# Performance work log

Measured on AMD Instinct MI355X. Metric: run time of the kernel, lower is better.

## Reference

```python
import jax, jax.numpy as jnp
import numpy as np

N, F_IN, F_OUT = 2048, 128, 64


def setup_inputs() -> dict:
    key = jax.random.key(0)
    k0, k1, k2, k3, k4 = jax.random.split(key, 5)
    node_features = jax.random.normal(k0, (N, F_IN), dtype=jnp.float32)
    adjacency_matrix = jax.random.uniform(k1, (N, N), dtype=jnp.float32)
    mask_father = jax.random.uniform(k2, (N, N), dtype=jnp.float32)
    mask_hadamard = jax.random.uniform(k3, (N, N), dtype=jnp.float32)
    # kaiming_uniform (fan_in, relu): bound = sqrt(6 / fan_in) * sqrt(2) adjustment -> gain*sqrt(3/fan_in)
    bound = np.sqrt(2.0) * np.sqrt(3.0 / F_IN)
    weight = jax.random.uniform(k4, (F_IN, F_OUT), dtype=jnp.float32, minval=-bound, maxval=bound)
    bias = jnp.zeros((F_OUT,), dtype=jnp.float32)
    return {
        "node_features": node_features,
        "adjacency_matrix": adjacency_matrix,
        "mask_father": mask_father,
        "mask_hadamard": mask_hadamard,
        "weight": weight,
        "bias": bias,
    }


def reference(node_features, adjacency_matrix, mask_father, mask_hadamard, weight, bias):
    # H[i,f] = (X @ W + b)[i,f]
    H = node_features @ weight + bias  # [N, F]
    # Original math: out[j,f] = sum_k mf[j,k] * H[k,f] * (sum_i A[j,i] * H[i,f] * mh[i,k])
    # G[j,f,k] corresponds to the (masked hadamard @ adjacency) intermediate [N, F, N]
    G = jnp.einsum('ji,if,ik->jfk', adjacency_matrix, H, mask_hadamard)
    out = jnp.einsum('jfk,kf,jk->jf', G, H, mask_father)
    return out
```

## Files before the change

### kernel.cpp

```cpp
#include <hip/hip_runtime.h>
#include <hip/hip_bf16.h>


typedef __attribute__((ext_vector_type(8))) _Float16 f16x8;
typedef __attribute__((ext_vector_type(4))) _Float16 f16x4;
typedef __attribute__((ext_vector_type(16))) float f32x16;

#define N 2048
#define FOUT 64
#define FIN 128
#define NIT 512

#define ZERO16 ((f32x16){0.f,0.f,0.f,0.f,0.f,0.f,0.f,0.f,0.f,0.f,0.f,0.f,0.f,0.f,0.f,0.f})
#define MFMA32(A,B,C) __builtin_amdgcn_mfma_f32_32x32x16_f16((A),(B),(C),0,0,0)

__device__ __forceinline__ void gl_lds16(const _Float16* g, _Float16* l) {
    __builtin_amdgcn_global_load_lds(
        (const __attribute__((address_space(1))) void*)g,
        (__attribute__((address_space(3))) void*)l, 16, 0, 0);
}


__global__ __launch_bounds__(256) void k_h(const float* __restrict__ X,
                                           const float* __restrict__ W,
                                           const float* __restrict__ bias,
                                           float* __restrict__ HT,
                                           _Float16* __restrict__ HTh) {
    __shared__ float Ws[FIN * FOUT];
    __shared__ float Xs[4 * FIN];
    int t = threadIdx.x;
#pragma unroll
    for (int s = 0; s < 32; ++s) Ws[t + 256 * s] = W[t + 256 * s];
    int i0 = blockIdx.x * 4;
#pragma unroll
    for (int s = 0; s < 2; ++s) { int idx = t + 256 * s; Xs[idx] = X[(size_t)i0 * FIN + idx]; }
    __syncthreads();
    int f = t & 63, il = t >> 6;
    float h = bias[f];
#pragma unroll
    for (int p = 0; p < FIN; ++p) h = fmaf(Xs[il * FIN + p], Ws[p * FOUT + f], h);
    int i = i0 + il;
    HT[f * N + i] = h;
    HTh[f * N + i] = (_Float16)h;
}

__global__ __launch_bounds__(256) void k_a2h(const float* __restrict__ A,
                                             _Float16* __restrict__ Ah) {
    int g = blockIdx.x * 256 + threadIdx.x;
    float4 v = ((const float4*)A)[g];
    f16x4 o;
    o[0] = (_Float16)v.x; o[1] = (_Float16)v.y; o[2] = (_Float16)v.z; o[3] = (_Float16)v.w;
    ((f16x4*)Ah)[g] = o;
}

__global__ __launch_bounds__(256) void k_mht(const float* __restrict__ mh,
                                             _Float16* __restrict__ mhT) {
    __shared__ float tile[64][65];
    int t = threadIdx.x;
    int bx = blockIdx.x & 31;
    int by = blockIdx.x >> 5;
#pragma unroll
    for (int s = 0; s < 16; ++s) {
        int lin = t + 256 * s;
        int r = lin >> 6, c = lin & 63;
        tile[r][c] = mh[(size_t)(by * 64 + r) * N + bx * 64 + c];
    }
    __syncthreads();
#pragma unroll
    for (int s = 0; s < 16; ++s) {
        int lin = t + 256 * s;
        int kr = lin >> 6, ic = lin & 63;
        mhT[(size_t)(bx * 64 + kr) * N + by * 64 + ic] = (_Float16)tile[ic][kr];
    }
}


#define STAGE(DBUF, IT)                                                        \
  {                                                                            \
    int ib_ = ((IT) & 31) << 6;                                                \
    int kt_ = (IT) >> 5;                                                       \
    const char* gA_ = (const char*)Ah + ((size_t)jbase * N + ib_) * 2;         \
    const char* gB_ = (const char*)mhT + ((size_t)kt_ * 128 * N + ib_) * 2;    \
    _Float16* la_ = &tiles[DBUF][0][lds_w];                                    \
    _Float16* lb_ = &tiles[DBUF][1][lds_w];                                    \
    _Pragma("unroll")                                                          \
    for (int c_ = 0; c_ < 4; ++c_) {                                           \
      gl_lds16((const _Float16*)(gA_ + (size_t)c_ * (16 * N) + vbyte), la_ + c_ * 512); \
      gl_lds16((const _Float16*)(gB_ + (size_t)c_ * (16 * N) + vbyte), lb_ + c_ * 512); \
    }                                                                          \
  }

#define COMPUTE_HALF(BUF, IT)                                                  \
  {                                                                            \
    const char* hb_ = (const char*)hbuf + ((((IT) & 31) << 6) * 2);            \
    __builtin_amdgcn_s_setprio(1);                                             \
    _Pragma("unroll")                                                          \
    for (int ks = 0; ks < 4; ++ks) {                                           \
      f16x8 a0 = *(const f16x8*)(tbase + addrA[ks] + (BUF) * 32768);           \
      f16x8 a1 = *(const f16x8*)(tbase + addrA[ks] + (BUF) * 32768 + 4096);    \
      f16x8 b0 = *(const f16x8*)(tbase + addrB[ks] + (BUF) * 32768 + 16384);   \
      f16x8 b1 = *(const f16x8*)(tbase + addrB[ks] + (BUF) * 32768 + 20480);   \
      f16x8 h0 = *(const f16x8*)(hb_ + hlb + ks * 32);                         \
      f16x8 h1 = *(const f16x8*)(hb_ + hlb + 4096 + ks * 32);                  \
      f16x8 a00 = a0 * h0, a10 = a1 * h0, a01 = a0 * h1, a11 = a1 * h1;        \
      acc[0][0][0] = MFMA32(a00, b0, acc[0][0][0]);                            \
      acc[0][0][1] = MFMA32(a00, b1, acc[0][0][1]);                            \
      acc[0][1][0] = MFMA32(a10, b0, acc[0][1][0]);                            \
      acc[0][1][1] = MFMA32(a10, b1, acc[0][1][1]);                            \
      acc[1][0][0] = MFMA32(a01, b0, acc[1][0][0]);                            \
      acc[1][0][1] = MFMA32(a01, b1, acc[1][0][1]);                            \
      acc[1][1][0] = MFMA32(a11, b0, acc[1][1][0]);                            \
      acc[1][1][1] = MFMA32(a11, b1, acc[1][1][1]);                            \
    }                                                                          \
    __builtin_amdgcn_s_setprio(0);                                             \
  }

#define EPILOGUE(IT)                                                           \
  {                                                                            \
    int kb_ = (((IT) >> 5) << 7) + wk;                                         \
    float hk0[2], hk1[2];                                                      \
    _Pragma("unroll")                                                          \
    for (int tk = 0; tk < 2; ++tk) {                                           \
      int kg = kb_ + tk * 32 + l31;                                            \
      hk0[tk] = HT[f0 * N + kg];                                               \
      hk1[tk] = HT[(f0 + 1) * N + kg];                                         \
    }                                                                          \
    _Pragma("unroll")                                                          \
    for (int tj = 0; tj < 2; ++tj) {                                           \
      int jr0 = jbase + wj + tj * 32 + hi * 4;                                 \
      _Pragma("unroll")                                                        \
      for (int r = 0; r < 16; ++r) {                                           \
        int jr = jr0 + (r & 3) + 8 * (r >> 2);                                 \
        float s0 = 0.f, s1 = 0.f;                                              \
        _Pragma("unroll")                                                      \
        for (int tk = 0; tk < 2; ++tk) {                                       \
          int kg = kb_ + tk * 32 + l31;                                        \
          float m = mf[(size_t)jr * N + kg];                                   \
          s0 = fmaf(acc[0][tj][tk][r], m * hk0[tk], s0);                       \
          s1 = fmaf(acc[1][tj][tk][r], m * hk1[tk], s1);                       \
        }                                                                      \
        s0 += __shfl_xor(s0, 1);  s1 += __shfl_xor(s1, 1);                     \
        s0 += __shfl_xor(s0, 2);  s1 += __shfl_xor(s1, 2);                     \
        s0 += __shfl_xor(s0, 4);  s1 += __shfl_xor(s1, 4);                     \
        s0 += __shfl_xor(s0, 8);  s1 += __shfl_xor(s1, 8);                     \
        s0 += __shfl_xor(s0, 16); s1 += __shfl_xor(s1, 16);                    \
        if (l31 == 0) {                                                        \
          int slot = tj * 32 + (r & 3) + 8 * (r >> 2) + 4 * hi;                \
          red[0][w][slot] += s0;                                               \
          red[1][w][slot] += s1;                                               \
        }                                                                      \
      }                                                                        \
    }                                                                          \
    _Pragma("unroll")                                                          \
    for (int f_ = 0; f_ < 2; ++f_)                                             \
      _Pragma("unroll")                                                        \
      for (int a_ = 0; a_ < 2; ++a_)                                           \
        _Pragma("unroll")                                                      \
        for (int b_ = 0; b_ < 2; ++b_) acc[f_][a_][b_] = ZERO16;               \
  }

__global__ __launch_bounds__(256, 2) void k_main(const float* __restrict__ mf,
                                                 const float* __restrict__ HT,
                                                 const _Float16* __restrict__ HTh,
                                                 const _Float16* __restrict__ Ah,
                                                 const _Float16* __restrict__ mhT,
                                                 float* __restrict__ out) {
    __shared__ _Float16 tiles[2][2][128 * 64];
    __shared__ _Float16 hbuf[2][N];
    __shared__ float red[2][4][64];

    int t = threadIdx.x;
    int jbase = (blockIdx.x >> 5) << 7;
    int f0 = (blockIdx.x & 31) << 1;
    int w = t >> 6, lane = t & 63;
    int l31 = lane & 31, hi = lane >> 5, l7 = lane & 7;
    int wj = (w & 1) << 6, wk = (w >> 1) << 6;

#pragma unroll
    for (int s = 0; s < 2; ++s) {
        int idx = t + 256 * s;
        ((f16x8*)hbuf)[idx] = *(const f16x8*)&HTh[(size_t)(f0 + (idx >> 8)) * N + (idx & 255) * 8];
    }
    ((float*)red)[t] = 0.f;
    ((float*)red)[t + 256] = 0.f;

    int lrow = lane >> 3;
    int lchunk = (lane & 7) ^ lrow;
    int vbyte = ((w * 32 + lrow) * N + lchunk * 8) * 2;
    int lds_w = w * 2048;

    const char* tbase = (const char*)&tiles[0][0][0];
    int hlb = hi * 16;
    int addrA[4], addrB[4];
#pragma unroll
    for (int ks = 0; ks < 4; ++ks) {
        int chs = ((ks * 2 + hi) ^ l7) * 16;
        addrA[ks] = (wj + l31) * 128 + chs;
        addrB[ks] = (wk + l31) * 128 + chs;
    }

    STAGE(0, 0)

    f32x16 acc[2][2][2];
#pragma unroll
    for (int f_ = 0; f_ < 2; ++f_)
#pragma unroll
        for (int a_ = 0; a_ < 2; ++a_)
#pragma unroll
            for (int b_ = 0; b_ < 2; ++b_) acc[f_][a_][b_] = ZERO16;

    for (int tp = 0; tp < NIT / 2; ++tp) {
        int it0 = tp * 2;
        __syncthreads();
        STAGE(1, it0 + 1)
        COMPUTE_HALF(0, it0)
        __syncthreads();
        if (tp != NIT / 2 - 1) STAGE(0, it0 + 2)
        COMPUTE_HALF(1, it0 + 1)
        if (((it0 + 1) & 31) == 31) EPILOGUE(it0 + 1)
    }

    __syncthreads();
    if (t < 128) {
        int j = t;
#pragma unroll
        for (int fi = 0; fi < 2; ++fi) {
            float v = (j < 64) ? (red[fi][0][j] + red[fi][2][j])
                               : (red[fi][1][j - 64] + red[fi][3][j - 64]);
            out[(size_t)(jbase + j) * FOUT + f0 + fi] = v;
        }
    }
}

extern "C" void kernel_launch(void* const* d_in, const int* in_sizes, int n_in,
                              void* d_out, int out_size, void* d_ws, size_t ws_size,
                              hipStream_t stream) {
    const float* X    = (const float*)d_in[0];
    const float* A    = (const float*)d_in[1];
    const float* mf   = (const float*)d_in[2];
    const float* mh   = (const float*)d_in[3];
    const float* W    = (const float*)d_in[4];
    const float* bias = (const float*)d_in[5];
    float* out = (float*)d_out;

    float*    HT  = (float*)d_ws;
    _Float16* HTh = (_Float16*)((char*)d_ws + 524288);
    _Float16* Ah  = (_Float16*)((char*)d_ws + 1048576);
    _Float16* mhT = (_Float16*)((char*)d_ws + 1048576 + 8388608);

    k_h<<<N / 4, 256, 0, stream>>>(X, W, bias, HT, HTh);
    k_a2h<<<(N * N / 4) / 256, 256, 0, stream>>>(A, Ah);
    k_mht<<<(N / 64) * (N / 64), 256, 0, stream>>>(mh, mhT);
    k_main<<<16 * 32, 256, 0, stream>>>(mf, HT, HTh, Ah, mhT, out);
}
```

Measured before the change: 1.253 ms.

## Split k range across blocks with atomics and switch to 16x16x32 MFMA tiles

The main kernel's k dimension is split in half across twice as many blocks, and partial outputs are combined with atomicAdd into an output that a new kernel zeroes first. The inner loop moves from 32x32x16 MFMAs with 64-wide i tiles to 16x16x32 MFMAs with 32-wide i tiles, halving LDS tile size, and the swizzles and epilogue reduction are reworked to match. The goal is more blocks across the CUs and a lighter LDS footprint, at the cost of an extra launch, atomics, and more MFMA instructions per unit of work.

```diff
diff --git a/kernel.cpp b/kernel.cpp
--- a/kernel.cpp
+++ b/kernel.cpp
@@ -4,15 +4,14 @@
 
 typedef __attribute__((ext_vector_type(8))) _Float16 f16x8;
 typedef __attribute__((ext_vector_type(4))) _Float16 f16x4;
-typedef __attribute__((ext_vector_type(16))) float f32x16;
+typedef __attribute__((ext_vector_type(4))) float f32x4;
 
 #define N 2048
 #define FOUT 64
 #define FIN 128
 #define NIT 512
 
-#define ZERO16 ((f32x16){0.f,0.f,0.f,0.f,0.f,0.f,0.f,0.f,0.f,0.f,0.f,0.f,0.f,0.f,0.f,0.f})
-#define MFMA32(A,B,C) __builtin_amdgcn_mfma_f32_32x32x16_f16((A),(B),(C),0,0,0)
+#define MFMA16(A,B,C) __builtin_amdgcn_mfma_f32_16x16x32_f16((A),(B),(C),0,0,0)
 
 __device__ __forceinline__ void gl_lds16(const _Float16* g, _Float16* l) {
     __builtin_amdgcn_global_load_lds(
@@ -20,6 +19,10 @@
         (__attribute__((address_space(3))) void*)l, 16, 0, 0);
 }
 
+
+__global__ __launch_bounds__(256) void k_zero(float* __restrict__ out) {
+    ((float4*)out)[blockIdx.x * 256 + threadIdx.x] = make_float4(0.f, 0.f, 0.f, 0.f);
+}
 
 __global__ __launch_bounds__(256) void k_h(const float* __restrict__ X,
                                            const float* __restrict__ W,
@@ -77,86 +80,86 @@
 
 #define STAGE(DBUF, IT)                                                        \
   {                                                                            \
-    int ib_ = ((IT) & 31) << 6;                                                \
-    int kt_ = (IT) >> 5;                                                       \
-    const char* gA_ = (const char*)Ah + ((size_t)jbase * N + ib_) * 2;         \
-    const char* gB_ = (const char*)mhT + ((size_t)kt_ * 128 * N + ib_) * 2;    \
-    _Float16* la_ = &tiles[DBUF][0][lds_w];                                    \
-    _Float16* lb_ = &tiles[DBUF][1][lds_w];                                    \
-    _Pragma("unroll")                                                          \
-    for (int c_ = 0; c_ < 4; ++c_) {                                           \
-      gl_lds16((const _Float16*)(gA_ + (size_t)c_ * (16 * N) + vbyte), la_ + c_ * 512); \
-      gl_lds16((const _Float16*)(gB_ + (size_t)c_ * (16 * N) + vbyte), lb_ + c_ * 512); \
+    int ib_ = ((IT) & 63) << 5;                                                \
+    int kt_ = (IT) >> 6;                                                       \
+    const _Float16* pa_ = Ah + a_base + ib_;                                   \
+    const _Float16* pb_ = mhT + b_base + (size_t)kt_ * 128 * N + ib_;          \
+    _Float16* la_ = &tiles[DBUF][0][w * 1024];                                 \
+    _Float16* lb_ = &tiles[DBUF][1][w * 1024];                                 \
+    _Pragma("unroll")                                                          \
+    for (int c_ = 0; c_ < 2; ++c_) {                                           \
+      gl_lds16(pa_ + c_ * 16 * N, la_ + c_ * 512);                             \
+      gl_lds16(pb_ + c_ * 16 * N, lb_ + c_ * 512);                             \
     }                                                                          \
   }
 
 #define COMPUTE_HALF(BUF, IT)                                                  \
   {                                                                            \
-    const char* hb_ = (const char*)hbuf + ((((IT) & 31) << 6) * 2);            \
+    const char* hb_ = (const char*)hbuf + (((IT) & 63) << 6);                  \
+    f16x8 ar[4], br[4];                                                        \
+    _Pragma("unroll")                                                          \
+    for (int x_ = 0; x_ < 4; ++x_)                                             \
+      ar[x_] = *(const f16x8*)(tbase + (BUF) * 16384 + faA + x_ * 1024);       \
+    _Pragma("unroll")                                                          \
+    for (int x_ = 0; x_ < 4; ++x_)                                             \
+      br[x_] = *(const f16x8*)(tbase + (BUF) * 16384 + 8192 + faB + x_ * 1024);\
+    f16x8 h0 = *(const f16x8*)(hb_ + hq);                                      \
+    f16x8 h1 = *(const f16x8*)(hb_ + 4096 + hq);                               \
     __builtin_amdgcn_s_setprio(1);                                             \
     _Pragma("unroll")                                                          \
-    for (int ks = 0; ks < 4; ++ks) {                                           \
-      f16x8 a0 = *(const f16x8*)(tbase + addrA[ks] + (BUF) * 32768);           \
-      f16x8 a1 = *(const f16x8*)(tbase + addrA[ks] + (BUF) * 32768 + 4096);    \
-      f16x8 b0 = *(const f16x8*)(tbase + addrB[ks] + (BUF) * 32768 + 16384);   \
-      f16x8 b1 = *(const f16x8*)(tbase + addrB[ks] + (BUF) * 32768 + 20480);   \
-      f16x8 h0 = *(const f16x8*)(hb_ + hlb + ks * 32);                         \
-      f16x8 h1 = *(const f16x8*)(hb_ + hlb + 4096 + ks * 32);                  \
-      f16x8 a00 = a0 * h0, a10 = a1 * h0, a01 = a0 * h1, a11 = a1 * h1;        \
-      acc[0][0][0] = MFMA32(a00, b0, acc[0][0][0]);                            \
-      acc[0][0][1] = MFMA32(a00, b1, acc[0][0][1]);                            \
-      acc[0][1][0] = MFMA32(a10, b0, acc[0][1][0]);                            \
-      acc[0][1][1] = MFMA32(a10, b1, acc[0][1][1]);                            \
-      acc[1][0][0] = MFMA32(a01, b0, acc[1][0][0]);                            \
-      acc[1][0][1] = MFMA32(a01, b1, acc[1][0][1]);                            \
-      acc[1][1][0] = MFMA32(a11, b0, acc[1][1][0]);                            \
-      acc[1][1][1] = MFMA32(a11, b1, acc[1][1][1]);                            \
+    for (int jj = 0; jj < 4; ++jj) {                                           \
+      f16x8 a0 = ar[jj] * h0;                                                  \
+      f16x8 a1 = ar[jj] * h1;                                                  \
+      _Pragma("unroll")                                                        \
+      for (int kk = 0; kk < 4; ++kk) {                                         \
+        acc[0][jj][kk] = MFMA16(a0, br[kk], acc[0][jj][kk]);                   \
+        acc[1][jj][kk] = MFMA16(a1, br[kk], acc[1][jj][kk]);                   \
+      }                                                                        \
     }                                                                          \
     __builtin_amdgcn_s_setprio(0);                                             \
+    if (((IT) & 63) == 63) EPILOGUE(IT)                                        \
   }
 
 #define EPILOGUE(IT)                                                           \
   {                                                                            \
-    int kb_ = (((IT) >> 5) << 7) + wk;                                         \
-    float hk0[2], hk1[2];                                                      \
-    _Pragma("unroll")                                                          \
-    for (int tk = 0; tk < 2; ++tk) {                                           \
-      int kg = kb_ + tk * 32 + l31;                                            \
-      hk0[tk] = HT[f0 * N + kg];                                               \
-      hk1[tk] = HT[(f0 + 1) * N + kg];                                         \
+    int kb_ = khalf + (((IT) >> 6) << 7);                                      \
+    _Pragma("unroll")                                                          \
+    for (int jj = 0; jj < 4; ++jj) {                                           \
+      float t0[4] = {0.f, 0.f, 0.f, 0.f};                                      \
+      float t1[4] = {0.f, 0.f, 0.f, 0.f};                                      \
+      int jrow = jbase + wj + jj * 16 + q * 4;                                 \
+      _Pragma("unroll")                                                        \
+      for (int kk = 0; kk < 4; ++kk) {                                         \
+        int kg = kb_ + wk + kk * 16 + l16;                                     \
+        float hk0 = HT[f0 * N + kg];                                           \
+        float hk1 = HT[(f0 + 1) * N + kg];                                     \
+        _Pragma("unroll")                                                      \
+        for (int r = 0; r < 4; ++r) {                                          \
+          float m = mf[(size_t)(jrow + r) * N + kg];                           \
+          t0[r] = fmaf(acc[0][jj][kk][r], m * hk0, t0[r]);                     \
+          t1[r] = fmaf(acc[1][jj][kk][r], m * hk1, t1[r]);                     \
+        }                                                                      \
+      }                                                                        \
+      _Pragma("unroll")                                                        \
+      for (int r = 0; r < 4; ++r) {                                            \
+        float v0 = t0[r], v1 = t1[r];                                          \
+        v0 += __shfl_xor(v0, 1); v1 += __shfl_xor(v1, 1);                      \
+        v0 += __shfl_xor(v0, 2); v1 += __shfl_xor(v1, 2);                      \
+        v0 += __shfl_xor(v0, 4); v1 += __shfl_xor(v1, 4);                      \
+        v0 += __shfl_xor(v0, 8); v1 += __shfl_xor(v1, 8);                      \
+        if (l16 == 0) {                                                        \
+          red[0][w][jj * 16 + q * 4 + r] += v0;                                \
+          red[1][w][jj * 16 + q * 4 + r] += v1;                                \
+        }                                                                      \
+      }                                                                        \
     }                                                                          \
     _Pragma("unroll")                                                          \
-    for (int tj = 0; tj < 2; ++tj) {                                           \
-      int jr0 = jbase + wj + tj * 32 + hi * 4;                                 \
-      _Pragma("unroll")                                                        \
-      for (int r = 0; r < 16; ++r) {                                           \
-        int jr = jr0 + (r & 3) + 8 * (r >> 2);                                 \
-        float s0 = 0.f, s1 = 0.f;                                              \
-        _Pragma("unroll")                                                      \
-        for (int tk = 0; tk < 2; ++tk) {                                       \
-          int kg = kb_ + tk * 32 + l31;                                        \
-          float m = mf[(size_t)jr * N + kg];                                   \
-          s0 = fmaf(acc[0][tj][tk][r], m * hk0[tk], s0);                       \
-          s1 = fmaf(acc[1][tj][tk][r], m * hk1[tk], s1);                       \
-        }                                                                      \
-        s0 += __shfl_xor(s0, 1);  s1 += __shfl_xor(s1, 1);                     \
-        s0 += __shfl_xor(s0, 2);  s1 += __shfl_xor(s1, 2);                     \
-        s0 += __shfl_xor(s0, 4);  s1 += __shfl_xor(s1, 4);                     \
-        s0 += __shfl_xor(s0, 8);  s1 += __shfl_xor(s1, 8);                     \
-        s0 += __shfl_xor(s0, 16); s1 += __shfl_xor(s1, 16);                    \
-        if (l31 == 0) {                                                        \
-          int slot = tj * 32 + (r & 3) + 8 * (r >> 2) + 4 * hi;                \
-          red[0][w][slot] += s0;                                               \
-          red[1][w][slot] += s1;                                               \
-        }                                                                      \
-      }                                                                        \
-    }                                                                          \
-    _Pragma("unroll")                                                          \
-    for (int f_ = 0; f_ < 2; ++f_)                                             \
-      _Pragma("unroll")                                                        \
-      for (int a_ = 0; a_ < 2; ++a_)                                           \
-        _Pragma("unroll")                                                      \
-        for (int b_ = 0; b_ < 2; ++b_) acc[f_][a_][b_] = ZERO16;               \
+    for (int a_ = 0; a_ < 4; ++a_)                                             \
+      _Pragma("unroll")                                                        \
+      for (int b_ = 0; b_ < 4; ++b_) {                                         \
+        acc[0][a_][b_] = (f32x4){0.f, 0.f, 0.f, 0.f};                          \
+        acc[1][a_][b_] = (f32x4){0.f, 0.f, 0.f, 0.f};                          \
+      }                                                                        \
   }
 
 __global__ __launch_bounds__(256, 2) void k_main(const float* __restrict__ mf,
@@ -165,15 +168,15 @@
                                                  const _Float16* __restrict__ Ah,
                                                  const _Float16* __restrict__ mhT,
                                                  float* __restrict__ out) {
-    __shared__ _Float16 tiles[2][2][128 * 64];
+    __shared__ _Float16 tiles[2][2][128 * 32];
     __shared__ _Float16 hbuf[2][N];
     __shared__ float red[2][4][64];
 
     int t = threadIdx.x;
-    int jbase = (blockIdx.x >> 5) << 7;
-    int f0 = (blockIdx.x & 31) << 1;
-    int w = t >> 6, lane = t & 63;
-    int l31 = lane & 31, hi = lane >> 5, l7 = lane & 7;
+    int jbase = (blockIdx.x >> 6) << 7;
+    int f0 = ((blockIdx.x >> 1) & 31) << 1;
+    int khalf = (blockIdx.x & 1) << 10;
+    int w = t >> 6, lane = t & 63, q = lane >> 4, l16 = lane & 15;
     int wj = (w & 1) << 6, wk = (w >> 1) << 6;
 
 #pragma unroll
@@ -184,30 +187,26 @@
     ((float*)red)[t] = 0.f;
     ((float*)red)[t + 256] = 0.f;
 
-    int lrow = lane >> 3;
-    int lchunk = (lane & 7) ^ lrow;
-    int vbyte = ((w * 32 + lrow) * N + lchunk * 8) * 2;
-    int lds_w = w * 2048;
+    int chlog = (lane & 3) ^ ((lane >> 3) & 3);
+    size_t a_base = (size_t)(jbase + w * 32 + (lane >> 2)) * N + chlog * 8;
+    size_t b_base = (size_t)(khalf + w * 32 + (lane >> 2)) * N + chlog * 8;
 
     const char* tbase = (const char*)&tiles[0][0][0];
-    int hlb = hi * 16;
-    int addrA[4], addrB[4];
-#pragma unroll
-    for (int ks = 0; ks < 4; ++ks) {
-        int chs = ((ks * 2 + hi) ^ l7) * 16;
-        addrA[ks] = (wj + l31) * 128 + chs;
-        addrB[ks] = (wk + l31) * 128 + chs;
-    }
+    int chr = (q ^ ((l16 >> 1) & 3)) * 16;
+    int faA = (wj + l16) * 64 + chr;
+    int faB = (wk + l16) * 64 + chr;
+    int hq = q * 16;
 
     STAGE(0, 0)
 
-    f32x16 acc[2][2][2];
-#pragma unroll
-    for (int f_ = 0; f_ < 2; ++f_)
-#pragma unroll
-        for (int a_ = 0; a_ < 2; ++a_)
-#pragma unroll
-            for (int b_ = 0; b_ < 2; ++b_) acc[f_][a_][b_] = ZERO16;
+    f32x4 acc[2][4][4];
+#pragma unroll
+    for (int a = 0; a < 4; ++a)
+#pragma unroll
+        for (int b = 0; b < 4; ++b) {
+            acc[0][a][b] = (f32x4){0.f, 0.f, 0.f, 0.f};
+            acc[1][a][b] = (f32x4){0.f, 0.f, 0.f, 0.f};
+        }
 
     for (int tp = 0; tp < NIT / 2; ++tp) {
         int it0 = tp * 2;
@@ -217,7 +216,6 @@
         __syncthreads();
         if (tp != NIT / 2 - 1) STAGE(0, it0 + 2)
         COMPUTE_HALF(1, it0 + 1)
-        if (((it0 + 1) & 31) == 31) EPILOGUE(it0 + 1)
     }
 
     __syncthreads();
@@ -227,7 +225,7 @@
         for (int fi = 0; fi < 2; ++fi) {
             float v = (j < 64) ? (red[fi][0][j] + red[fi][2][j])
                                : (red[fi][1][j - 64] + red[fi][3][j - 64]);
-            out[(size_t)(jbase + j) * FOUT + f0 + fi] = v;
+            atomicAdd(&out[(size_t)(jbase + j) * FOUT + f0 + fi], v);
         }
     }
 }
@@ -248,8 +246,9 @@
     _Float16* Ah  = (_Float16*)((char*)d_ws + 1048576);
     _Float16* mhT = (_Float16*)((char*)d_ws + 1048576 + 8388608);
 
+    k_zero<<<(N * FOUT / 4) / 256, 256, 0, stream>>>(out);
     k_h<<<N / 4, 256, 0, stream>>>(X, W, bias, HT, HTh);
     k_a2h<<<(N * N / 4) / 256, 256, 0, stream>>>(A, Ah);
     k_mht<<<(N / 64) * (N / 64), 256, 0, stream>>>(mh, mhT);
-    k_main<<<16 * 32, 256, 0, stream>>>(mf, HT, HTh, Ah, mhT, out);
-}
+    k_main<<<16 * 32 * 2, 256, 0, stream>>>(mf, HT, HTh, Ah, mhT, out);
+}
```

Result: faster. 1.049 ms (-16.3%).

## Software-pipeline main loop with register double-buffered LDS reads and explicit waitcnt

Applied to the files above, without the earlier changes.

Restructures the main GEMM loop so LDS fragment reads for the next k-step are issued into a second register set while the current MFMAs run. The first fragment of the next tile is prefetched at the end of each iteration. The two barriers per iteration pair become one barrier per iteration, with manual s_waitcnt vmcnt and sched_barrier fencing around the async global-to-LDS copies. Shared memory is flattened into one byte array with hand-computed offsets. This is meant to hide LDS latency and barrier stalls behind MFMA work. The cost is more live registers and a risk of reading LDS data other waves have not finished loading, because only per-wave vmcnt waits guard the prefetch.

```diff
diff --git a/kernel.cpp b/kernel.cpp
--- a/kernel.cpp
+++ b/kernel.cpp
@@ -11,8 +11,13 @@
 #define FIN 128
 #define NIT 512
 
+#define MFMA32(A,B,C) __builtin_amdgcn_mfma_f32_32x32x16_f16((A),(B),(C),0,0,0)
+#define SB0 __builtin_amdgcn_sched_barrier(0);
+#define BARS { __builtin_amdgcn_s_barrier(); SB0 }
+#define VM8  { asm volatile("s_waitcnt vmcnt(8)" ::: "memory"); SB0 }
+#define VM0  { asm volatile("s_waitcnt vmcnt(0)" ::: "memory"); SB0 }
+
 #define ZERO16 ((f32x16){0.f,0.f,0.f,0.f,0.f,0.f,0.f,0.f,0.f,0.f,0.f,0.f,0.f,0.f,0.f,0.f})
-#define MFMA32(A,B,C) __builtin_amdgcn_mfma_f32_32x32x16_f16((A),(B),(C),0,0,0)
 
 __device__ __forceinline__ void gl_lds16(const _Float16* g, _Float16* l) {
     __builtin_amdgcn_global_load_lds(
@@ -75,44 +80,45 @@
 }
 
 
-#define STAGE(DBUF, IT)                                                        \
+#define TOFF(BUFL, AB) (10240 + (BUFL) * 32768 + (AB) * 16384)
+
+#define STAGE(IT, BUFL)                                                        \
   {                                                                            \
     int ib_ = ((IT) & 31) << 6;                                                \
     int kt_ = (IT) >> 5;                                                       \
-    const char* gA_ = (const char*)Ah + ((size_t)jbase * N + ib_) * 2;         \
-    const char* gB_ = (const char*)mhT + ((size_t)kt_ * 128 * N + ib_) * 2;    \
-    _Float16* la_ = &tiles[DBUF][0][lds_w];                                    \
-    _Float16* lb_ = &tiles[DBUF][1][lds_w];                                    \
+    const _Float16* pa_ = Ah + a_base + ib_;                                   \
+    const _Float16* pb_ = mhT + b_base + (size_t)kt_ * 128 * N + ib_;          \
+    _Float16* la_ = (_Float16*)(lds + TOFF(BUFL, 0) + wbyte);                  \
+    _Float16* lb_ = (_Float16*)(lds + TOFF(BUFL, 1) + wbyte);                  \
     _Pragma("unroll")                                                          \
     for (int c_ = 0; c_ < 4; ++c_) {                                           \
-      gl_lds16((const _Float16*)(gA_ + (size_t)c_ * (16 * N) + vbyte), la_ + c_ * 512); \
-      gl_lds16((const _Float16*)(gB_ + (size_t)c_ * (16 * N) + vbyte), lb_ + c_ * 512); \
-    }                                                                          \
-  }
-
-#define COMPUTE_HALF(BUF, IT)                                                  \
-  {                                                                            \
-    const char* hb_ = (const char*)hbuf + ((((IT) & 31) << 6) * 2);            \
-    __builtin_amdgcn_s_setprio(1);                                             \
-    _Pragma("unroll")                                                          \
-    for (int ks = 0; ks < 4; ++ks) {                                           \
-      f16x8 a0 = *(const f16x8*)(tbase + addrA[ks] + (BUF) * 32768);           \
-      f16x8 a1 = *(const f16x8*)(tbase + addrA[ks] + (BUF) * 32768 + 4096);    \
-      f16x8 b0 = *(const f16x8*)(tbase + addrB[ks] + (BUF) * 32768 + 16384);   \
-      f16x8 b1 = *(const f16x8*)(tbase + addrB[ks] + (BUF) * 32768 + 20480);   \
-      f16x8 h0 = *(const f16x8*)(hb_ + hlb + ks * 32);                         \
-      f16x8 h1 = *(const f16x8*)(hb_ + hlb + 4096 + ks * 32);                  \
-      f16x8 a00 = a0 * h0, a10 = a1 * h0, a01 = a0 * h1, a11 = a1 * h1;        \
-      acc[0][0][0] = MFMA32(a00, b0, acc[0][0][0]);                            \
-      acc[0][0][1] = MFMA32(a00, b1, acc[0][0][1]);                            \
-      acc[0][1][0] = MFMA32(a10, b0, acc[0][1][0]);                            \
-      acc[0][1][1] = MFMA32(a10, b1, acc[0][1][1]);                            \
-      acc[1][0][0] = MFMA32(a01, b0, acc[1][0][0]);                            \
-      acc[1][0][1] = MFMA32(a01, b1, acc[1][0][1]);                            \
-      acc[1][1][0] = MFMA32(a11, b0, acc[1][1][0]);                            \
-      acc[1][1][1] = MFMA32(a11, b1, acc[1][1][1]);                            \
-    }                                                                          \
-    __builtin_amdgcn_s_setprio(0);                                             \
+      gl_lds16(pa_ + c_ * 8 * N, la_ + c_ * 512);                              \
+      gl_lds16(pb_ + c_ * 8 * N, lb_ + c_ * 512);                              \
+    }                                                                          \
+  }
+
+#define READS(SUF, KS, BUFL, VH)                                               \
+  xA0##SUF = *(const f16x8*)(lds + TOFF(BUFL, 0) + vA0 + chnk[KS]);            \
+  xA1##SUF = *(const f16x8*)(lds + TOFF(BUFL, 0) + vA1 + chnk[KS]);            \
+  xB0##SUF = *(const f16x8*)(lds + TOFF(BUFL, 1) + vB0 + chnk[KS]);            \
+  xB1##SUF = *(const f16x8*)(lds + TOFF(BUFL, 1) + vB1 + chnk[KS]);            \
+  xH0##SUF = *(const f16x8*)(lds + (VH) + (KS) * 32);                          \
+  xH1##SUF = *(const f16x8*)(lds + (VH) + (KS) * 32 + 4096);
+
+#define MFMA8(SUF)                                                             \
+  {                                                                            \
+    f16x8 p00 = xA0##SUF * xH0##SUF;                                           \
+    f16x8 p10 = xA1##SUF * xH0##SUF;                                           \
+    f16x8 p01 = xA0##SUF * xH1##SUF;                                           \
+    f16x8 p11 = xA1##SUF * xH1##SUF;                                           \
+    acc[0][0][0] = MFMA32(p00, xB0##SUF, acc[0][0][0]);                        \
+    acc[0][0][1] = MFMA32(p00, xB1##SUF, acc[0][0][1]);                        \
+    acc[0][1][0] = MFMA32(p10, xB0##SUF, acc[0][1][0]);                        \
+    acc[0][1][1] = MFMA32(p10, xB1##SUF, acc[0][1][1]);                        \
+    acc[1][0][0] = MFMA32(p01, xB0##SUF, acc[1][0][0]);                        \
+    acc[1][0][1] = MFMA32(p01, xB1##SUF, acc[1][0][1]);                        \
+    acc[1][1][0] = MFMA32(p11, xB0##SUF, acc[1][1][0]);                        \
+    acc[1][1][1] = MFMA32(p11, xB1##SUF, acc[1][1][1]);                        \
   }
 
 #define EPILOGUE(IT)                                                           \
@@ -146,8 +152,8 @@
         s0 += __shfl_xor(s0, 16); s1 += __shfl_xor(s1, 16);                    \
         if (l31 == 0) {                                                        \
           int slot = tj * 32 + (r & 3) + 8 * (r >> 2) + 4 * hi;                \
-          red[0][w][slot] += s0;                                               \
-          red[1][w][slot] += s1;                                               \
+          redp[(0 * 4 + w) * 64 + slot] += s0;                                 \
+          redp[(1 * 4 + w) * 64 + slot] += s1;                                 \
         }                                                                      \
       }                                                                        \
     }                                                                          \
@@ -157,6 +163,27 @@
       for (int a_ = 0; a_ < 2; ++a_)                                           \
         _Pragma("unroll")                                                      \
         for (int b_ = 0; b_ < 2; ++b_) acc[f_][a_][b_] = ZERO16;               \
+  }
+
+#define ITER(IT, BUFL, DO_STAGE, DO_NEXT, VMW)                                 \
+  {                                                                            \
+    BARS                                                                       \
+    if (DO_STAGE) STAGE((IT) + 1, (BUFL) ^ 1)                                  \
+    VMW                                                                        \
+    int vh = vhb + (((IT) & 31) << 7);                                         \
+    READS(b, 1, BUFL, vh)                                                      \
+    MFMA8(a)                                                          \
+    READS(a, 2, BUFL, vh)                                                      \
+    MFMA8(b)                                                          \
+    READS(b, 3, BUFL, vh)                                                      \
+    MFMA8(a)                                                          \
+    if (DO_NEXT) {                                                             \
+      VM0                                                                      \
+      int vh2 = vhb + ((((IT) + 1) & 31) << 7);                                \
+      READS(a, 0, (BUFL) ^ 1, vh2)                 \
+    }                                                                          \
+    MFMA8(b)                                                          \
+    if (((IT) & 31) == 31) EPILOGUE(IT)                                        \
   }
 
 __global__ __launch_bounds__(256, 2) void k_main(const float* __restrict__ mf,
@@ -165,9 +192,8 @@
                                                  const _Float16* __restrict__ Ah,
                                                  const _Float16* __restrict__ mhT,
                                                  float* __restrict__ out) {
-    __shared__ _Float16 tiles[2][2][128 * 64];
-    __shared__ _Float16 hbuf[2][N];
-    __shared__ float red[2][4][64];
+    __shared__ __align__(16) char lds[75776];
+    float* redp = (float*)(lds + 8192);
 
     int t = threadIdx.x;
     int jbase = (blockIdx.x >> 5) << 7;
@@ -179,54 +205,55 @@
 #pragma unroll
     for (int s = 0; s < 2; ++s) {
         int idx = t + 256 * s;
-        ((f16x8*)hbuf)[idx] = *(const f16x8*)&HTh[(size_t)(f0 + (idx >> 8)) * N + (idx & 255) * 8];
-    }
-    ((float*)red)[t] = 0.f;
-    ((float*)red)[t + 256] = 0.f;
+        ((f16x8*)lds)[idx] = *(const f16x8*)&HTh[(size_t)(f0 + (idx >> 8)) * N + (idx & 255) * 8];
+    }
+    redp[t] = 0.f;
+    redp[t + 256] = 0.f;
 
     int lrow = lane >> 3;
     int lchunk = (lane & 7) ^ lrow;
-    int vbyte = ((w * 32 + lrow) * N + lchunk * 8) * 2;
-    int lds_w = w * 2048;
-
-    const char* tbase = (const char*)&tiles[0][0][0];
-    int hlb = hi * 16;
-    int addrA[4], addrB[4];
-#pragma unroll
-    for (int ks = 0; ks < 4; ++ks) {
-        int chs = ((ks * 2 + hi) ^ l7) * 16;
-        addrA[ks] = (wj + l31) * 128 + chs;
-        addrB[ks] = (wk + l31) * 128 + chs;
-    }
+    int a_base = (jbase + w * 32 + lrow) * N + lchunk * 8;
+    int b_base = (w * 32 + lrow) * N + lchunk * 8;
+    int wbyte = w * 4096;
+
+    int vA0 = (wj + 0 + l31) * 128;
+    int vA1 = (wj + 32 + l31) * 128;
+    int vB0 = (wk + 0 + l31) * 128;
+    int vB1 = (wk + 32 + l31) * 128;
+    int chnk[4];
+#pragma unroll
+    for (int ks = 0; ks < 4; ++ks) chnk[ks] = ((ks * 2 + hi) ^ l7) * 16;
+    int vhb = hi * 16;
+
+    f16x8 xA0a, xA1a, xB0a, xB1a, xH0a, xH1a;
+    f16x8 xA0b, xA1b, xB0b, xB1b, xH0b, xH1b;
+
+    f32x16 acc[2][2][2];
+#pragma unroll
+    for (int f_ = 0; f_ < 2; ++f_)
+#pragma unroll
+        for (int a_ = 0; a_ < 2; ++a_)
+#pragma unroll
+            for (int b_ = 0; b_ < 2; ++b_) acc[f_][a_][b_] = ZERO16;
 
     STAGE(0, 0)
-
-    f32x16 acc[2][2][2];
-#pragma unroll
-    for (int f_ = 0; f_ < 2; ++f_)
-#pragma unroll
-        for (int a_ = 0; a_ < 2; ++a_)
-#pragma unroll
-            for (int b_ = 0; b_ < 2; ++b_) acc[f_][a_][b_] = ZERO16;
-
-    for (int tp = 0; tp < NIT / 2; ++tp) {
-        int it0 = tp * 2;
-        __syncthreads();
-        STAGE(1, it0 + 1)
-        COMPUTE_HALF(0, it0)
-        __syncthreads();
-        if (tp != NIT / 2 - 1) STAGE(0, it0 + 2)
-        COMPUTE_HALF(1, it0 + 1)
-        if (((it0 + 1) & 31) == 31) EPILOGUE(it0 + 1)
-    }
+    __syncthreads();
+    READS(a, 0, 0, vhb)
+
+    for (int tp = 0; tp < 255; ++tp) {
+        ITER(tp * 2,     0, 1, 1, VM8)
+        ITER(tp * 2 + 1, 1, 1, 1, VM8)
+    }
+    ITER(510, 0, 1, 1, VM8)
+    ITER(511, 1, 0, 0, VM0)
 
     __syncthreads();
     if (t < 128) {
         int j = t;
 #pragma unroll
         for (int fi = 0; fi < 2; ++fi) {
-            float v = (j < 64) ? (red[fi][0][j] + red[fi][2][j])
-                               : (red[fi][1][j - 64] + red[fi][3][j - 64]);
+            float v = (j < 64) ? (redp[(fi * 4 + 0) * 64 + j] + redp[(fi * 4 + 2) * 64 + j])
+                               : (redp[(fi * 4 + 1) * 64 + j - 64] + redp[(fi * 4 + 3) * 64 + j - 64]);
             out[(size_t)(jbase + j) * FOUT + f0 + fi] = v;
         }
     }
```

New measurement: 1.176 ms. -6.1%, faster.
